# Optimization experiments

Hardware: AMD Instinct MI355X
Metric: run time of the kernel (lower is better)

## Reference

```python
import jax, jax.numpy as jnp
import numpy as np

B, S, D, H, L, TPB = 4, 1020, 1024, 16, 4, 17
VOBS, VACT = 4096, 16
DH = D // H
EPS = 1e-3  # keras LayerNormalization default epsilon


def _ln(x, g, b):
    m = jnp.mean(x, axis=-1, keepdims=True)
    v = jnp.mean((x - m) ** 2, axis=-1, keepdims=True)
    return (x - m) * jax.lax.rsqrt(v + EPS) * g + b


def setup_inputs() -> dict:
    key = jax.random.key(0)
    ks = iter(jax.random.split(key, 64))
    def p(shape, s=0.02):
        return jax.random.normal(next(ks), shape, jnp.float32) * s
    pos = np.arange(S)
    is_obs = jnp.asarray((pos % TPB) < (TPB - 1))
    tok = jax.random.randint(next(ks), (B, S), 0, VOBS)
    tok = jnp.where(is_obs[None, :], tok, tok % VACT).astype(jnp.int32)
    d = dict(
        tokens=tok,
        pos_emb=p((S, D)), emb_obs=p((VOBS, D)), emb_act=p((VACT, D)),
        ln1_g=jnp.ones((L, D)), ln1_b=jnp.zeros((L, D)),
        wq=p((L, D, D)), bq=jnp.zeros((L, D)),
        wk=p((L, D, D)), bk=jnp.zeros((L, D)),
        wv=p((L, D, D)), bv=jnp.zeros((L, D)),
        wo=p((L, D, D)), bo=jnp.zeros((L, D)),
        ln2_g=jnp.ones((L, D)), ln2_b=jnp.zeros((L, D)),
        w1=p((L, D, 4 * D)), b1=jnp.zeros((L, 4 * D)),
        w2=p((L, 4 * D, D)), b2=jnp.zeros((L, D)),
        lnf_g=jnp.ones((D,)), lnf_b=jnp.zeros((D,)),
        ho1=p((D, D)), bo1=jnp.zeros((D,)),
        ho2=p((D, VOBS)), bo2=jnp.zeros((VOBS,)),
        he1=p((D, D)), be1=jnp.zeros((D,)),
        he2=p((D, 2)), be2=jnp.zeros((2,)),
    )
    return d


def reference(tokens, pos_emb, emb_obs, emb_act, ln1_g, ln1_b, wq, bq, wk, bk,
              wv, bv, wo, bo, ln2_g, ln2_b, w1, b1, w2, b2, lnf_g, lnf_b,
              ho1, bo1, ho2, bo2, he1, be1, he2, be2):
    pos = jnp.arange(S)
    is_obs = (pos % TPB) < (TPB - 1)  # obs positions within each block
    # token embedding: obs table on obs positions, act table on act positions
    x = jnp.where(is_obs[None, :, None],
                  emb_obs[jnp.minimum(tokens, VOBS - 1)],
                  emb_act[jnp.minimum(tokens, VACT - 1)])
    x = x + pos_emb[None]
    neg_mask = (1.0 - jnp.tril(jnp.ones((S, S), jnp.float32))) * -1e9
    inv_sqrt_dk = 1.0 / np.sqrt(DH).astype(np.float32)
    for i in range(L):
        h = _ln(x, ln1_g[i], ln1_b[i])
        q = (h @ wq[i] + bq[i]).reshape(B, S, H, DH).transpose(0, 2, 1, 3)
        k = (h @ wk[i] + bk[i]).reshape(B, S, H, DH).transpose(0, 2, 1, 3)
        v = (h @ wv[i] + bv[i]).reshape(B, S, H, DH).transpose(0, 2, 1, 3)
        scores = jnp.einsum('bhqd,bhkd->bhqk', q, k) * inv_sqrt_dk + neg_mask
        w = jax.nn.softmax(scores, axis=-1)
        o = jnp.einsum('bhqk,bhkd->bhqd', w, v).transpose(0, 2, 1, 3).reshape(B, S, D)
        x = x + (o @ wo[i] + bo[i])
        h = _ln(x, ln2_g[i], ln2_b[i])
        h = jax.nn.gelu(h @ w1[i] + b1[i], approximate=False) @ w2[i] + b2[i]
        x = x + h
    x = _ln(x, lnf_g, lnf_b)
    # head slices (static)
    p_np = np.arange(S)
    head_obs_idx = jnp.asarray(np.nonzero(((p_np + 1) % TPB) != (TPB - 1))[0])  # 960
    act_idx = jnp.asarray(np.nonzero((p_np % TPB) == (TPB - 1))[0])            # 60
    xo = x[:, head_obs_idx]
    logits_obs = jax.nn.relu(xo @ ho1 + bo1) @ ho2 + bo2   # [B, 960, VOBS]
    xe = x[:, act_idx]
    logits_ends = jax.nn.relu(xe @ he1 + be1) @ he2 + be2  # [B, 60, 2]
    return (logits_obs, logits_ends)
```

## Files before the change

kernel.cpp:

```cpp
#include <hip/hip_runtime.h>
#include <hip/hip_bf16.h>
#include <math.h>

namespace {

constexpr int kS = 1020, kD = 1024, kTPB = 17, kDH = 64;
constexpr int kVOBS = 4096, kVACT = 16;
constexpr int kBS = 4080;
constexpr float kEPS = 1e-3f;

typedef float f32x4 __attribute__((ext_vector_type(4)));
typedef __bf16 bfx8 __attribute__((ext_vector_type(8)));
typedef unsigned short u16;
typedef u16 us8 __attribute__((ext_vector_type(8)));
typedef u16 us4 __attribute__((ext_vector_type(4)));

__device__ __forceinline__ float bf2f(u16 u) {
  union { unsigned int i; float f; } v; v.i = (unsigned int)u << 16; return v.f;
}
__device__ __forceinline__ u16 f2bf(float f) {
  union { float f; unsigned int i; } v; v.f = f;
  unsigned int r = v.i + 0x7FFFu + ((v.i >> 16) & 1u);
  return (u16)(r >> 16);
}

__global__ void k_embed(const int* __restrict__ tokens, const float* __restrict__ pos_emb,
                        const float* __restrict__ emb_obs, const float* __restrict__ emb_act,
                        float* __restrict__ x) {
  int bs = blockIdx.x;
  int s = bs % kS;
  int tk = tokens[bs];
  bool obs = (s % kTPB) < (kTPB - 1);
  const float* e;
  if (obs) { int t2 = tk < kVOBS - 1 ? tk : kVOBS - 1; e = emb_obs + (size_t)t2 * kD; }
  else     { int t2 = tk < kVACT - 1 ? tk : kVACT - 1; e = emb_act + (size_t)t2 * kD; }
  int c = threadIdx.x * 4;
  float4 ev = *(const float4*)(e + c);
  float4 pv = *(const float4*)(pos_emb + (size_t)s * kD + c);
  float4 o; o.x = ev.x + pv.x; o.y = ev.y + pv.y; o.z = ev.z + pv.z; o.w = ev.w + pv.w;
  *(float4*)(x + (size_t)bs * kD + c) = o;
}

__global__ void k_pack_bias(const float* __restrict__ bq, const float* __restrict__ bk,
                            const float* __restrict__ bv, float* __restrict__ bqkv) {
  int idx = blockIdx.x * 256 + threadIdx.x;
  int l = idx / 3072, rem = idx % 3072;
  int sel = rem >> 10, cc = rem & 1023;
  const float* src = sel == 0 ? bq : (sel == 1 ? bk : bv);
  bqkv[idx] = src[l * kD + cc];
}

__global__ void k_ln(const float* __restrict__ x, const float* __restrict__ g,
                     const float* __restrict__ b, u16* __restrict__ out) {
  int row = blockIdx.x;
  int t = threadIdx.x;
  const float* xr = x + (size_t)row * kD;
  float4 v = *(const float4*)(xr + t * 4);
  float s1 = v.x + v.y + v.z + v.w;
  float s2 = v.x * v.x + v.y * v.y + v.z * v.z + v.w * v.w;
  #pragma unroll
  for (int m = 32; m; m >>= 1) { s1 += __shfl_xor(s1, m); s2 += __shfl_xor(s2, m); }
  __shared__ float ls1[4], ls2[4];
  int w = t >> 6;
  if ((t & 63) == 0) { ls1[w] = s1; ls2[w] = s2; }
  __syncthreads();
  float S1 = ls1[0] + ls1[1] + ls1[2] + ls1[3];
  float S2 = ls2[0] + ls2[1] + ls2[2] + ls2[3];
  float mean = S1 * (1.0f / kD);
  float var = S2 * (1.0f / kD) - mean * mean;
  float rs = rsqrtf(var + kEPS);
  int c = t * 4;
  float4 gv = *(const float4*)(g + c);
  float4 bv = *(const float4*)(b + c);
  us4 o;
  o[0] = f2bf((v.x - mean) * rs * gv.x + bv.x);
  o[1] = f2bf((v.y - mean) * rs * gv.y + bv.y);
  o[2] = f2bf((v.z - mean) * rs * gv.z + bv.z);
  o[3] = f2bf((v.w - mean) * rs * gv.w + bv.w);
  *(us4*)(out + (size_t)row * kD + c) = o;
}

__global__ void k_transpose(const float* __restrict__ in, u16* __restrict__ out,
                            int R, int C, int ld) {
  __shared__ float tile[32][33];
  int tx = threadIdx.x, ty = threadIdx.y;
  int c0 = blockIdx.x * 32, r0 = blockIdx.y * 32;
  #pragma unroll
  for (int i = 0; i < 4; ++i)
    tile[ty + i * 8][tx] = in[(size_t)(r0 + ty + i * 8) * ld + c0 + tx];
  __syncthreads();
  #pragma unroll
  for (int i = 0; i < 4; ++i)
    out[(size_t)(c0 + ty + i * 8) * R + r0 + tx] = f2bf(tile[tx][ty + i * 8]);
}

template <int EPI, int BM>
__global__ void __launch_bounds__(256)
k_gemm(const u16* __restrict__ A, const u16* __restrict__ Bt, const float* __restrict__ bias,
       const float* __restrict__ resid, void* __restrict__ out, int M, int N, int K, int ldo) {
  constexpr int MFRAG = BM / 32;
  __shared__ alignas(16) u16 As[2][BM * 32];
  __shared__ alignas(16) u16 Bs[2][128 * 32];
  int tid = threadIdx.x;
  int m0 = blockIdx.x * BM, n0 = blockIdx.y * 128;
  int lane = tid & 63, wv = tid >> 6;
  int wm = wv >> 1, wn = wv & 1;
  f32x4 acc[MFRAG][4] = {};

  auto stage = [&](int buf, int k0) {
    #pragma unroll
    for (int n = 0; n < BM / 64; ++n) {
      int u = n * 256 + tid;
      int r = u >> 2, ch = u & 3;
      int gr = m0 + r; if (gr >= M) gr = M - 1;
      int cg = ch ^ ((r >> 1) & 3);
      const u16* src = A + (size_t)gr * K + k0 + cg * 8;
      __builtin_amdgcn_global_load_lds(
          (const __attribute__((address_space(1))) unsigned int*)src,
          (__attribute__((address_space(3))) unsigned int*)&As[buf][(n * 256 + wv * 64) * 8],
          16, 0, 0);
    }
    #pragma unroll
    for (int n = 0; n < 2; ++n) {
      int u = n * 256 + tid;
      int r = u >> 2, ch = u & 3;
      int cg = ch ^ ((r >> 1) & 3);
      const u16* src = Bt + (size_t)(n0 + r) * K + k0 + cg * 8;
      __builtin_amdgcn_global_load_lds(
          (const __attribute__((address_space(1))) unsigned int*)src,
          (__attribute__((address_space(3))) unsigned int*)&Bs[buf][(n * 256 + wv * 64) * 8],
          16, 0, 0);
    }
  };

  stage(0, 0);
  __syncthreads();
  const int nk = K >> 5;
  for (int t = 0; t < nk; ++t) {
    int cur = t & 1;
    if (t + 1 < nk) stage(cur ^ 1, (t + 1) << 5);

    bfx8 af[MFRAG], bfr[4];
    int ch = lane >> 4;
    #pragma unroll
    for (int mf = 0; mf < MFRAG; ++mf) {
      int row = wm * (BM / 2) + mf * 16 + (lane & 15);
      af[mf] = *(const bfx8*)(&As[cur][row * 32 + ((ch ^ ((row >> 1) & 3)) << 3)]);
    }
    #pragma unroll
    for (int nf = 0; nf < 4; ++nf) {
      int row = wn * 64 + nf * 16 + (lane & 15);
      bfr[nf] = *(const bfx8*)(&Bs[cur][row * 32 + ((ch ^ ((row >> 1) & 3)) << 3)]);
    }
    #pragma unroll
    for (int mf = 0; mf < MFRAG; ++mf)
      #pragma unroll
      for (int nf = 0; nf < 4; ++nf)
        acc[mf][nf] = __builtin_amdgcn_mfma_f32_16x16x32_bf16(af[mf], bfr[nf], acc[mf][nf], 0, 0, 0);
    __syncthreads();
  }

  #pragma unroll
  for (int mf = 0; mf < MFRAG; ++mf) {
    #pragma unroll
    for (int nf = 0; nf < 4; ++nf) {
      int gcol = n0 + wn * 64 + nf * 16 + (lane & 15);
      float bv = bias ? bias[gcol] : 0.0f;
      #pragma unroll
      for (int r = 0; r < 4; ++r) {
        int grow = m0 + wm * (BM / 2) + mf * 16 + (lane >> 4) * 4 + r;
        if (grow >= M) continue;
        float val = acc[mf][nf][r] + bv;
        size_t off2 = (size_t)grow * ldo + gcol;
        if (EPI == 0) {
          ((u16*)out)[off2] = f2bf(val);
        } else if (EPI == 1) {
          ((u16*)out)[off2] = f2bf(val > 0.f ? val : 0.f);
        } else if (EPI == 2) {
          ((u16*)out)[off2] = f2bf(0.5f * val * (1.f + erff(val * 0.70710678118654752440f)));
        } else if (EPI == 3) {
          ((float*)out)[off2] = resid[off2] + val;
        } else {
          ((float*)out)[off2] = val;
        }
      }
    }
  }
}

__device__ __forceinline__ int swz(int row, int colu16) {
  return (row * 64 + colu16) ^ ((row & 7) << 3) ^ ((row & 24) << 1);
}

__global__ void __launch_bounds__(256)
k_attn(const u16* __restrict__ q, const u16* __restrict__ k, const u16* __restrict__ v,
       u16* __restrict__ o, int ldin) {
  __shared__ u16 Kl[64 * 64];
  __shared__ u16 Vt[64 * 64];
  const int qb = blockIdx.x * 64;
  const int bh = blockIdx.y;
  const int b = bh >> 4, hh = bh & 15;
  const int tid = threadIdx.x;
  const int lane = tid & 63, w = tid >> 6;
  const int g = lane >> 4, c = lane & 15;
  const int q0 = qb + w * 16;
  const size_t base = (size_t)(b * kS) * ldin + hh * kDH;

  bfx8 qf0, qf1;
  {
    int qr = q0 + c; if (qr >= kS) qr = kS - 1;
    const u16* qp = q + base + (size_t)qr * ldin + g * 8;
    qf0 = *(const bfx8*)(qp);
    qf1 = *(const bfx8*)(qp + 32);
  }

  float mst = -1e30f, lsum = 0.f;
  f32x4 ot[4] = {};

  const int ntiles = blockIdx.x + 1;
  for (int t = 0; t < ntiles; ++t) {
    const int kt = t * 64;
    {
      int kr = tid >> 2, ds2 = (tid & 3) * 16;
      int kg = kt + kr; if (kg >= kS) kg = kS - 1;
      const u16* kp = k + base + (size_t)kg * ldin + ds2;
      us8 a0 = *(const us8*)(kp);
      us8 a1 = *(const us8*)(kp + 8);
      *(us8*)(&Kl[swz(kr, ds2)]) = a0;
      *(us8*)(&Kl[swz(kr, ds2 + 8)]) = a1;
      const u16* vp = v + base + (size_t)kg * ldin + ds2;
      us8 b0 = *(const us8*)(vp);
      us8 b1 = *(const us8*)(vp + 8);
      #pragma unroll
      for (int i2 = 0; i2 < 8; ++i2) Vt[swz(ds2 + i2, kr)] = b0[i2];
      #pragma unroll
      for (int i2 = 0; i2 < 8; ++i2) Vt[swz(ds2 + 8 + i2, kr)] = b1[i2];
    }
    __syncthreads();

    f32x4 s[4];
    #pragma unroll
    for (int kb = 0; kb < 4; ++kb) {
      bfx8 kf0 = *(const bfx8*)(&Kl[swz(kb * 16 + c, g * 8)]);
      bfx8 kf1 = *(const bfx8*)(&Kl[swz(kb * 16 + c, g * 8 + 32)]);
      f32x4 acc = {};
      acc = __builtin_amdgcn_mfma_f32_16x16x32_bf16(kf0, qf0, acc, 0, 0, 0);
      acc = __builtin_amdgcn_mfma_f32_16x16x32_bf16(kf1, qf1, acc, 0, 0, 0);
      s[kb] = acc;
    }

    const int qg = q0 + c;
    const bool diag = (kt + 63 > q0);
    float p[4][4];
    float tmax = -1e30f;
    #pragma unroll
    for (int kb = 0; kb < 4; ++kb)
      #pragma unroll
      for (int r = 0; r < 4; ++r) {
        float val = s[kb][r] * 0.125f;
        if (diag && (kt + kb * 16 + g * 4 + r > qg)) val = -1e30f;
        p[kb][r] = val;
        tmax = fmaxf(tmax, val);
      }
    tmax = fmaxf(tmax, __shfl_xor(tmax, 16));
    tmax = fmaxf(tmax, __shfl_xor(tmax, 32));
    float mnew = fmaxf(mst, tmax);
    float alpha = __expf(mst - mnew);
    float psum = 0.f;
    #pragma unroll
    for (int kb = 0; kb < 4; ++kb)
      #pragma unroll
      for (int r = 0; r < 4; ++r) {
        float e = __expf(p[kb][r] - mnew);
        p[kb][r] = e;
        psum += e;
      }
    psum += __shfl_xor(psum, 16);
    psum += __shfl_xor(psum, 32);
    lsum = lsum * alpha + psum;
    mst = mnew;
    #pragma unroll
    for (int db = 0; db < 4; ++db) {
      ot[db][0] *= alpha; ot[db][1] *= alpha;
      ot[db][2] *= alpha; ot[db][3] *= alpha;
    }

    #pragma unroll
    for (int h = 0; h < 2; ++h) {
      bfx8 pf;
      #pragma unroll
      for (int j = 0; j < 8; ++j)
        pf[j] = (__bf16)p[2 * h + (j >> 2)][j & 3];
      #pragma unroll
      for (int db = 0; db < 4; ++db) {
        us4 lo = *(const us4*)(&Vt[swz(16 * db + c, 32 * h + 4 * g)]);
        us4 hi = *(const us4*)(&Vt[swz(16 * db + c, 32 * h + 16 + 4 * g)]);
        union { us8 u; bfx8 bf; } cv;
        cv.u[0] = lo[0]; cv.u[1] = lo[1]; cv.u[2] = lo[2]; cv.u[3] = lo[3];
        cv.u[4] = hi[0]; cv.u[5] = hi[1]; cv.u[6] = hi[2]; cv.u[7] = hi[3];
        ot[db] = __builtin_amdgcn_mfma_f32_16x16x32_bf16(cv.bf, pf, ot[db], 0, 0, 0);
      }
    }
    __syncthreads();
  }

  if (q0 + c < kS) {
    float inv = 1.0f / lsum;
    u16* op = o + (size_t)(b * kS) * kD + hh * kDH + (size_t)(q0 + c) * kD;
    #pragma unroll
    for (int db = 0; db < 4; ++db)
      #pragma unroll
      for (int r = 0; r < 4; ++r)
        op[16 * db + 4 * g + r] = f2bf(ot[db][r] * inv);
  }
}

__global__ void k_gather_obs(const u16* __restrict__ xf, u16* __restrict__ xo) {
  int r = blockIdx.x;
  int b = r / 960, rr = r % 960;
  int j = rr & 15, blk = rr >> 4;
  int s = blk * kTPB + j + (j == 15 ? 1 : 0);
  const unsigned int* src = (const unsigned int*)(xf + ((size_t)(b * kS + s)) * kD);
  unsigned int* dst = (unsigned int*)(xo + (size_t)r * kD);
  dst[threadIdx.x] = src[threadIdx.x];
  dst[threadIdx.x + 256] = src[threadIdx.x + 256];
}
__global__ void k_gather_act(const u16* __restrict__ xf, u16* __restrict__ xe) {
  int r = blockIdx.x;
  int b = r / 60, rr = r % 60;
  int s = rr * kTPB + (kTPB - 1);
  const unsigned int* src = (const unsigned int*)(xf + ((size_t)(b * kS + s)) * kD);
  unsigned int* dst = (unsigned int*)(xe + (size_t)r * kD);
  dst[threadIdx.x] = src[threadIdx.x];
  dst[threadIdx.x + 256] = src[threadIdx.x + 256];
}

__global__ void k_ends(const u16* __restrict__ t2, const float* __restrict__ he2,
                       const float* __restrict__ be2, float* __restrict__ out) {
  int r = blockIdx.x;
  int t = threadIdx.x;
  float p0 = 0.f, p1 = 0.f;
  for (int j = t; j < kD; j += 256) {
    float xv = bf2f(t2[(size_t)r * kD + j]);
    p0 += xv * he2[j * 2];
    p1 += xv * he2[j * 2 + 1];
  }
  #pragma unroll
  for (int msk = 32; msk; msk >>= 1) { p0 += __shfl_xor(p0, msk); p1 += __shfl_xor(p1, msk); }
  __shared__ float l0[4], l1[4];
  int w = t >> 6;
  if ((t & 63) == 0) { l0[w] = p0; l1[w] = p1; }
  __syncthreads();
  if (t == 0) {
    out[r * 2 + 0] = l0[0] + l0[1] + l0[2] + l0[3] + be2[0];
    out[r * 2 + 1] = l1[0] + l1[1] + l1[2] + l1[3] + be2[1];
  }
}

}

extern "C" void kernel_launch(void* const* d_in, const int* in_sizes, int n_in,
                              void* d_out, int out_size, void* d_ws, size_t ws_size,
                              hipStream_t stream) {
  const int*   tokens  = (const int*)  d_in[0];
  const float* pos_emb = (const float*)d_in[1];
  const float* emb_obs = (const float*)d_in[2];
  const float* emb_act = (const float*)d_in[3];
  const float* ln1_g = (const float*)d_in[4];
  const float* ln1_b = (const float*)d_in[5];
  const float* wq = (const float*)d_in[6];
  const float* bq = (const float*)d_in[7];
  const float* wk = (const float*)d_in[8];
  const float* bk = (const float*)d_in[9];
  const float* wv = (const float*)d_in[10];
  const float* bv = (const float*)d_in[11];
  const float* wo = (const float*)d_in[12];
  const float* bo = (const float*)d_in[13];
  const float* ln2_g = (const float*)d_in[14];
  const float* ln2_b = (const float*)d_in[15];
  const float* w1 = (const float*)d_in[16];
  const float* b1 = (const float*)d_in[17];
  const float* w2 = (const float*)d_in[18];
  const float* b2 = (const float*)d_in[19];
  const float* lnf_g = (const float*)d_in[20];
  const float* lnf_b = (const float*)d_in[21];
  const float* ho1 = (const float*)d_in[22];
  const float* bo1 = (const float*)d_in[23];
  const float* ho2 = (const float*)d_in[24];
  const float* bo2 = (const float*)d_in[25];
  const float* he1 = (const float*)d_in[26];
  const float* be1 = (const float*)d_in[27];
  const float* he2 = (const float*)d_in[28];
  const float* be2 = (const float*)d_in[29];
  (void)in_sizes; (void)n_in; (void)out_size; (void)ws_size;

  char* ws = (char*)d_ws;
  size_t off = 0;
  auto alloc = [&](size_t bytes) -> char* {
    char* p = ws + off; off += (bytes + 255) & ~(size_t)255; return p;
  };
  u16*   wTbig = (u16*)alloc((size_t)4096 * 1024 * 2);
  float* x  = (float*)alloc((size_t)kBS * kD * 4);
  u16*   h  = (u16*)alloc((size_t)kBS * kD * 2);
  char*  scr = alloc((size_t)kBS * 4096 * 2);
  float* bqkv = (float*)alloc((size_t)4 * 3072 * 4);
  const size_t slotB = (size_t)kBS * kD * 2;
  u16* qkv = (u16*)scr;
  u16* ob  = (u16*)(scr + (size_t)kBS * 3072 * 2);
  u16* mid = (u16*)scr;
  u16* xf = (u16*)scr;
  u16* xo = (u16*)(scr + slotB);
  u16* t1 = (u16*)(scr + 2 * slotB);
  u16* xe = (u16*)(scr + 3 * slotB);
  u16* t2 = (u16*)(scr + 3 * slotB + (size_t)240 * kD * 2 + 256);

  dim3 tb(32, 8);
  dim3 tg(32, 32);
  k_embed<<<kBS, 256, 0, stream>>>(tokens, pos_emb, emb_obs, emb_act, x);
  k_pack_bias<<<48, 256, 0, stream>>>(bq, bk, bv, bqkv);

  for (int i = 0; i < 4; ++i) {
    const size_t wOff = (size_t)i * kD * kD;
    k_ln<<<kBS, 256, 0, stream>>>(x, ln1_g + i * kD, ln1_b + i * kD, h);

    k_transpose<<<tg, tb, 0, stream>>>(wq + wOff, wTbig, 1024, 1024, 1024);
    k_transpose<<<tg, tb, 0, stream>>>(wk + wOff, wTbig + (size_t)1024 * 1024, 1024, 1024, 1024);
    k_transpose<<<tg, tb, 0, stream>>>(wv + wOff, wTbig + (size_t)2048 * 1024, 1024, 1024, 1024);
    k_gemm<0, 128><<<dim3(32, 24), 256, 0, stream>>>(h, wTbig, bqkv + i * 3072, nullptr, qkv,
                                                     kBS, 3072, 1024, 3072);

    k_attn<<<dim3(16, 64), 256, 0, stream>>>(qkv, qkv + 1024, qkv + 2048, ob, 3072);

    k_transpose<<<tg, tb, 0, stream>>>(wo + wOff, wTbig, 1024, 1024, 1024);
    k_gemm<3, 64><<<dim3(64, 8), 256, 0, stream>>>(ob, wTbig, bo + i * kD, x, x,
                                                   kBS, 1024, 1024, 1024);

    k_ln<<<kBS, 256, 0, stream>>>(x, ln2_g + i * kD, ln2_b + i * kD, h);

    for (int c = 0; c < 4; ++c)
      k_transpose<<<tg, tb, 0, stream>>>(w1 + (size_t)i * kD * 4096 + c * 1024,
                                         wTbig + (size_t)c * 1024 * 1024, 1024, 1024, 4096);
    k_gemm<2, 128><<<dim3(32, 32), 256, 0, stream>>>(h, wTbig, b1 + (size_t)i * 4096, nullptr,
                                                     mid, kBS, 4096, 1024, 4096);
    k_transpose<<<dim3(32, 128), tb, 0, stream>>>(w2 + (size_t)i * 4096 * kD, wTbig,
                                                  4096, 1024, 1024);
    k_gemm<3, 64><<<dim3(64, 8), 256, 0, stream>>>(mid, wTbig, b2 + i * kD, x, x,
                                                   kBS, 1024, 4096, 1024);
  }

  k_ln<<<kBS, 256, 0, stream>>>(x, lnf_g, lnf_b, xf);
  k_gather_obs<<<3840, 256, 0, stream>>>(xf, xo);
  k_gather_act<<<240, 256, 0, stream>>>(xf, xe);

  k_transpose<<<tg, tb, 0, stream>>>(ho1, wTbig, 1024, 1024, 1024);
  k_gemm<1, 64><<<dim3(60, 8), 256, 0, stream>>>(xo, wTbig, bo1, nullptr, t1,
                                                 3840, 1024, 1024, 1024);
  for (int c = 0; c < 4; ++c)
    k_transpose<<<tg, tb, 0, stream>>>(ho2 + c * 1024, wTbig + (size_t)c * 1024 * 1024,
                                       1024, 1024, 4096);
  k_gemm<4, 128><<<dim3(30, 32), 256, 0, stream>>>(t1, wTbig, bo2, nullptr,
                                                   (float*)d_out, 3840, 4096, 1024, 4096);
  k_transpose<<<tg, tb, 0, stream>>>(he1, wTbig, 1024, 1024, 1024);
  k_gemm<1, 64><<<dim3(4, 8), 256, 0, stream>>>(xe, wTbig, be1, nullptr, t2,
                                                240, 1024, 1024, 1024);
  k_ends<<<240, 256, 0, stream>>>(t2, he2, be2, (float*)d_out + (size_t)3840 * 4096);
}
```

Baseline: 1.377 ms.

## Triple-buffer GEMM K-loop with vmcnt waits and batch weight transposes

The GEMM main loop moves from double to triple buffering in LDS. It prefetches two K-tiles ahead, waits with explicit s_waitcnt vmcnt counts instead of a full sync, and issues the next stage right after the fragment loads so the loads overlap the MFMAs. Separately, the per-chunk weight transpose launches are merged into one 4-way batched kernel, and W2/he1 get their own buffer so fewer launches are needed. The extra LDS buffer raises shared memory use per block, which may lower occupancy, and the hand-written waitcnt logic must match the exact number of loads per stage.

```diff
diff --git a/kernel.cpp b/kernel.cpp
--- a/kernel.cpp
+++ b/kernel.cpp
@@ -94,13 +94,39 @@
     out[(size_t)(c0 + ty + i * 8) * R + r0 + tx] = f2bf(tile[tx][ty + i * 8]);
 }
 
+struct T4 {
+  const float* in0; const float* in1; const float* in2; const float* in3;
+  u16* out0; u16* out1; u16* out2; u16* out3;
+  int ld;
+};
+__global__ void k_transpose4(T4 sp) {
+  const float* in; u16* out;
+  switch (blockIdx.z) {
+    case 0:  in = sp.in0; out = sp.out0; break;
+    case 1:  in = sp.in1; out = sp.out1; break;
+    case 2:  in = sp.in2; out = sp.out2; break;
+    default: in = sp.in3; out = sp.out3; break;
+  }
+  __shared__ float tile[32][33];
+  int tx = threadIdx.x, ty = threadIdx.y;
+  int c0 = blockIdx.x * 32, r0 = blockIdx.y * 32;
+  #pragma unroll
+  for (int i = 0; i < 4; ++i)
+    tile[ty + i * 8][tx] = in[(size_t)(r0 + ty + i * 8) * sp.ld + c0 + tx];
+  __syncthreads();
+  #pragma unroll
+  for (int i = 0; i < 4; ++i)
+    out[(size_t)(c0 + ty + i * 8) * 1024 + r0 + tx] = f2bf(tile[tx][ty + i * 8]);
+}
+
 template <int EPI, int BM>
 __global__ void __launch_bounds__(256)
 k_gemm(const u16* __restrict__ A, const u16* __restrict__ Bt, const float* __restrict__ bias,
        const float* __restrict__ resid, void* __restrict__ out, int M, int N, int K, int ldo) {
   constexpr int MFRAG = BM / 32;
-  __shared__ alignas(16) u16 As[2][BM * 32];
-  __shared__ alignas(16) u16 Bs[2][128 * 32];
+  constexpr int LOADS = BM / 64 + 2;
+  __shared__ alignas(16) u16 As[3][BM * 32];
+  __shared__ alignas(16) u16 Bs[3][128 * 32];
   int tid = threadIdx.x;
   int m0 = blockIdx.x * BM, n0 = blockIdx.y * 128;
   int lane = tid & 63, wv = tid >> 6;
@@ -133,12 +159,20 @@
     }
   };
 
+  const int nk = K >> 5;
   stage(0, 0);
-  __syncthreads();
-  const int nk = K >> 5;
+  stage(1, 32);
+  stage(2, 64);
   for (int t = 0; t < nk; ++t) {
-    int cur = t & 1;
-    if (t + 1 < nk) stage(cur ^ 1, (t + 1) << 5);
+    int cur = t % 3;
+    if (t + 2 < nk)
+      asm volatile("s_waitcnt vmcnt(%0)" :: "i"(2 * LOADS) : "memory");
+    else if (t + 1 < nk)
+      asm volatile("s_waitcnt vmcnt(%0)" :: "i"(LOADS) : "memory");
+    else
+      asm volatile("s_waitcnt vmcnt(0)" ::: "memory");
+    __builtin_amdgcn_s_barrier();
+    __builtin_amdgcn_sched_barrier(0);
 
     bfx8 af[MFRAG], bfr[4];
     int ch = lane >> 4;
@@ -152,12 +186,16 @@
       int row = wn * 64 + nf * 16 + (lane & 15);
       bfr[nf] = *(const bfx8*)(&Bs[cur][row * 32 + ((ch ^ ((row >> 1) & 3)) << 3)]);
     }
+    asm volatile("s_waitcnt lgkmcnt(0)" ::: "memory");
+    __builtin_amdgcn_s_barrier();
+    __builtin_amdgcn_sched_barrier(0);
+    if (t + 3 < nk) stage(cur, (t + 3) << 5);
+
     #pragma unroll
     for (int mf = 0; mf < MFRAG; ++mf)
       #pragma unroll
       for (int nf = 0; nf < 4; ++nf)
         acc[mf][nf] = __builtin_amdgcn_mfma_f32_16x16x32_bf16(af[mf], bfr[nf], acc[mf][nf], 0, 0, 0);
-    __syncthreads();
   }
 
   #pragma unroll
@@ -400,6 +438,7 @@
     char* p = ws + off; off += (bytes + 255) & ~(size_t)255; return p;
   };
   u16*   wTbig = (u16*)alloc((size_t)4096 * 1024 * 2);
+  u16*   w2T   = (u16*)alloc((size_t)1024 * 4096 * 2);
   float* x  = (float*)alloc((size_t)kBS * kD * 4);
   u16*   h  = (u16*)alloc((size_t)kBS * kD * 2);
   char*  scr = alloc((size_t)kBS * 4096 * 2);
@@ -419,32 +458,37 @@
   k_embed<<<kBS, 256, 0, stream>>>(tokens, pos_emb, emb_obs, emb_act, x);
   k_pack_bias<<<48, 256, 0, stream>>>(bq, bk, bv, bqkv);
 
+  const size_t MB1 = (size_t)1024 * 1024;
   for (int i = 0; i < 4; ++i) {
     const size_t wOff = (size_t)i * kD * kD;
     k_ln<<<kBS, 256, 0, stream>>>(x, ln1_g + i * kD, ln1_b + i * kD, h);
 
-    k_transpose<<<tg, tb, 0, stream>>>(wq + wOff, wTbig, 1024, 1024, 1024);
-    k_transpose<<<tg, tb, 0, stream>>>(wk + wOff, wTbig + (size_t)1024 * 1024, 1024, 1024, 1024);
-    k_transpose<<<tg, tb, 0, stream>>>(wv + wOff, wTbig + (size_t)2048 * 1024, 1024, 1024, 1024);
+    {
+      T4 sp{wq + wOff, wk + wOff, wv + wOff, wo + wOff,
+            wTbig, wTbig + MB1, wTbig + 2 * MB1, wTbig + 3 * MB1, 1024};
+      k_transpose4<<<dim3(32, 32, 4), tb, 0, stream>>>(sp);
+    }
     k_gemm<0, 128><<<dim3(32, 24), 256, 0, stream>>>(h, wTbig, bqkv + i * 3072, nullptr, qkv,
                                                      kBS, 3072, 1024, 3072);
 
     k_attn<<<dim3(16, 64), 256, 0, stream>>>(qkv, qkv + 1024, qkv + 2048, ob, 3072);
 
-    k_transpose<<<tg, tb, 0, stream>>>(wo + wOff, wTbig, 1024, 1024, 1024);
-    k_gemm<3, 64><<<dim3(64, 8), 256, 0, stream>>>(ob, wTbig, bo + i * kD, x, x,
+    k_gemm<3, 64><<<dim3(64, 8), 256, 0, stream>>>(ob, wTbig + 3 * MB1, bo + i * kD, x, x,
                                                    kBS, 1024, 1024, 1024);
 
     k_ln<<<kBS, 256, 0, stream>>>(x, ln2_g + i * kD, ln2_b + i * kD, h);
 
-    for (int c = 0; c < 4; ++c)
-      k_transpose<<<tg, tb, 0, stream>>>(w1 + (size_t)i * kD * 4096 + c * 1024,
-                                         wTbig + (size_t)c * 1024 * 1024, 1024, 1024, 4096);
+    {
+      const float* w1b = w1 + (size_t)i * kD * 4096;
+      T4 sp{w1b, w1b + 1024, w1b + 2048, w1b + 3072,
+            wTbig, wTbig + MB1, wTbig + 2 * MB1, wTbig + 3 * MB1, 4096};
+      k_transpose4<<<dim3(32, 32, 4), tb, 0, stream>>>(sp);
+    }
+    k_transpose<<<dim3(32, 128), tb, 0, stream>>>(w2 + (size_t)i * 4096 * kD, w2T,
+                                                  4096, 1024, 1024);
     k_gemm<2, 128><<<dim3(32, 32), 256, 0, stream>>>(h, wTbig, b1 + (size_t)i * 4096, nullptr,
                                                      mid, kBS, 4096, 1024, 4096);
-    k_transpose<<<dim3(32, 128), tb, 0, stream>>>(w2 + (size_t)i * 4096 * kD, wTbig,
-                                                  4096, 1024, 1024);
-    k_gemm<3, 64><<<dim3(64, 8), 256, 0, stream>>>(mid, wTbig, b2 + i * kD, x, x,
+    k_gemm<3, 64><<<dim3(64, 8), 256, 0, stream>>>(mid, w2T, b2 + i * kD, x, x,
                                                    kBS, 1024, 4096, 1024);
   }
 
@@ -455,13 +499,15 @@
   k_transpose<<<tg, tb, 0, stream>>>(ho1, wTbig, 1024, 1024, 1024);
   k_gemm<1, 64><<<dim3(60, 8), 256, 0, stream>>>(xo, wTbig, bo1, nullptr, t1,
                                                  3840, 1024, 1024, 1024);
-  for (int c = 0; c < 4; ++c)
-    k_transpose<<<tg, tb, 0, stream>>>(ho2 + c * 1024, wTbig + (size_t)c * 1024 * 1024,
-                                       1024, 1024, 4096);
+  k_transpose<<<tg, tb, 0, stream>>>(he1, w2T, 1024, 1024, 1024);
+  {
+    T4 sp{ho2, ho2 + 1024, ho2 + 2048, ho2 + 3072,
+          wTbig, wTbig + MB1, wTbig + 2 * MB1, wTbig + 3 * MB1, 4096};
+    k_transpose4<<<dim3(32, 32, 4), tb, 0, stream>>>(sp);
+  }
   k_gemm<4, 128><<<dim3(30, 32), 256, 0, stream>>>(t1, wTbig, bo2, nullptr,
                                                    (float*)d_out, 3840, 4096, 1024, 4096);
-  k_transpose<<<tg, tb, 0, stream>>>(he1, wTbig, 1024, 1024, 1024);
-  k_gemm<1, 64><<<dim3(4, 8), 256, 0, stream>>>(xe, wTbig, be1, nullptr, t2,
+  k_gemm<1, 64><<<dim3(4, 8), 256, 0, stream>>>(xe, w2T, be1, nullptr, t2,
                                                 240, 1024, 1024, 1024);
   k_ends<<<240, 256, 0, stream>>>(t2, he2, be2, (float*)d_out + (size_t)3840 * 4096);
 }
```

After: 1.283 ms. 6.9% less time.
